# Kernel optimization log

Hardware: AMD Instinct MI355X
Metric: run time of the kernel (lower is better)

The kernel has to match this reference:

```python
import jax, jax.numpy as jnp
import numpy as np

B, S, E, H, DK = 2, 1024, 1024, 128, 8  # batch, seq, embed_dim, num_heads, d_k (= n_wires)


def setup_inputs() -> dict:
    key = jax.random.key(0)
    ks = jax.random.split(key, 10)
    sc = 1.0 / np.sqrt(E)
    inp = {
        "x": jax.random.normal(ks[0], (B, S, E), dtype=jnp.float32),
        "Wq": jax.random.normal(ks[1], (E, E), dtype=jnp.float32) * sc,
        "bq": jnp.zeros((E,), jnp.float32),
        "Wk": jax.random.normal(ks[2], (E, E), dtype=jnp.float32) * sc,
        "bk": jnp.zeros((E,), jnp.float32),
        "Wv": jax.random.normal(ks[3], (E, E), dtype=jnp.float32) * sc,
        "bv": jnp.zeros((E,), jnp.float32),
        "phi": jax.random.uniform(ks[4], (H, DK), jnp.float32, -np.pi, np.pi),  # trainable RX angles per head
        "Wo": jax.random.normal(ks[5], (E, E), dtype=jnp.float32) * sc,
        "bo": jnp.zeros((E,), jnp.float32),
    }
    return inp


def reference(x, Wq, bq, Wk, bk, Wv, bv, phi, Wo, bo):
    b, s, e = x.shape
    h, dk = phi.shape
    # QKV projections (k, v are computed but unused in the original forward)
    q = (x @ Wq.T + bq).reshape(b, s, h, dk).transpose(0, 2, 1, 3)  # [B,H,S,DK]
    k = (x @ Wk.T + bk).reshape(b, s, h, dk).transpose(0, 2, 1, 3)
    v = (x @ Wv.T + bv).reshape(b, s, h, dk).transpose(0, 2, 1, 3)
    del k, v  # dead in original math
    # Quantum circuit per head: RX(q_i) then RX(phi_i) on |0>, measure PauliZ.
    # RX angles on same wire add; <Z> after RX(theta)|0> = cos(theta).
    out = jnp.cos(q + phi[None, :, None, :])  # [B,H,S,DK]
    scores = jnp.einsum("bhsd,bhtd->bhst", out, out) / np.sqrt(dk)
    attn = jax.nn.softmax(scores, axis=-1)  # dropout is identity in eval mode
    ctx = jnp.einsum("bhst,bhtd->bhsd", attn, out)
    ctx = ctx.transpose(0, 2, 1, 3).reshape(b, s, e)
    return ctx @ Wo.T + bo
```

## Files before the change

kernel.cpp:

```cpp
#include <hip/hip_runtime.h>
#include <hip/hip_bf16.h>

#define Bv  2
#define Sv  1024
#define Ev  1024
#define Hv  128
#define DKv 8
#define Mv  (Bv*Sv)

typedef __attribute__((ext_vector_type(8))) short short8;
typedef __attribute__((ext_vector_type(4))) float f32x4;

static __device__ __forceinline__ short f2b(float f) {
    __hip_bfloat16 h = __float2bfloat16(f);
    return *reinterpret_cast<short*>(&h);
}

static __device__ __forceinline__ unsigned cvtpk(float a, float b) {
    unsigned r;
    asm("v_cvt_pk_bf16_f32 %0, %1, %2" : "=v"(r) : "v"(a), "v"(b));
    return r;
}

static __device__ __forceinline__ float hexp2(float x) {
    return __builtin_amdgcn_exp2f(x);
}

static __device__ __forceinline__ void gload16(const void* g, void* l) {
    __builtin_amdgcn_global_load_lds(
        (const __attribute__((address_space(1))) unsigned int*)g,
        (__attribute__((address_space(3))) unsigned int*)l, 16, 0, 0);
}

__global__ __launch_bounds__(256)
void cvt_all(const float* __restrict__ x, const float* __restrict__ wq,
             const float* __restrict__ wo, short* __restrict__ xb,
             short* __restrict__ wqb, short* __restrict__ wob)
{
    const int b = blockIdx.x;
    const float* src; short* dst; int i;
    if (b < 1024)      { src = x;  dst = xb;  i = b * 256 + threadIdx.x; }
    else if (b < 1536) { src = wq; dst = wqb; i = (b - 1024) * 256 + threadIdx.x; }
    else               { src = wo; dst = wob; i = (b - 1536) * 256 + threadIdx.x; }
    float4 a = ((const float4*)src)[2 * i];
    float4 c = ((const float4*)src)[2 * i + 1];
    uint4 o;
    o.x = cvtpk(a.x, a.y); o.y = cvtpk(a.z, a.w);
    o.z = cvtpk(c.x, c.y); o.w = cvtpk(c.z, c.w);
    ((uint4*)dst)[i] = o;
}

template<int EPI>
__global__ __launch_bounds__(256)
void gemm_bf16(const short* __restrict__ A, const short* __restrict__ W,
               const float* __restrict__ bias, const float* __restrict__ phi,
               void* __restrict__ outv)
{
    __shared__ short As[2][64 * 64];
    __shared__ short Bs[2][64 * 64];

    const int t    = threadIdx.x;
    const int w    = t >> 6, lane = t & 63;
    const int c    = lane & 15, g = lane >> 4;
    const int cs   = c & 7;
    const int wr   = w >> 1,  wc = w & 1;
    const int tm   = blockIdx.y * 64, tn = blockIdx.x * 64;
    const int lr   = lane >> 3;
    const int lcs  = ((lane & 7) ^ lr) * 8;

    f32x4 acc[2][2] = {};

    #define STAGE(s, k0)                                                        \
        _Pragma("unroll")                                                       \
        for (int j = 0; j < 2; j++) {                                           \
            const int row = w * 16 + j * 8;                                     \
            gload16(&A[(size_t)(tm + row + lr) * Ev + (k0) + lcs], &As[s][row * 64]); \
            gload16(&W[(size_t)(tn + row + lr) * Ev + (k0) + lcs], &Bs[s][row * 64]); \
        }

    STAGE(0, 0)
    __syncthreads();

    for (int ks = 0; ks < 16; ks++) {
        const int cur = ks & 1;
        if (ks < 15) { STAGE(cur ^ 1, (ks + 1) * 64) }
        #pragma unroll
        for (int kk = 0; kk < 64; kk += 32) {
            const int s0 = ((kk >> 3) + g) ^ cs;
            short8 af[2], bf[2];
            #pragma unroll
            for (int m = 0; m < 2; m++)
                af[m] = *(const short8*)&As[cur][(wr * 32 + m * 16 + c) * 64 + s0 * 8];
            #pragma unroll
            for (int n = 0; n < 2; n++)
                bf[n] = *(const short8*)&Bs[cur][(wc * 32 + n * 16 + c) * 64 + s0 * 8];
            #pragma unroll
            for (int m = 0; m < 2; m++)
                #pragma unroll
                for (int n = 0; n < 2; n++)
                    acc[m][n] = __builtin_amdgcn_mfma_f32_16x16x32_bf16(af[m], bf[n], acc[m][n], 0, 0, 0);
        }
        __syncthreads();
    }

    #pragma unroll
    for (int i = 0; i < 2; i++) {
        #pragma unroll
        for (int j = 0; j < 2; j++) {
            const int n = tn + wc * 32 + j * 16 + c;
            #pragma unroll
            for (int r = 0; r < 4; r++) {
                const int m = tm + wr * 32 + i * 16 + 4 * g + r;
                const float v = acc[i][j][r];
                if (EPI == 0) {
                    float q = __cosf(v + bias[n] + phi[n]);
                    const int bb = m >> 10, ss = m & (Sv - 1);
                    const int hh = n >> 3,  dd = n & (DKv - 1);
                    ((short*)outv)[(((size_t)bb * Hv + hh) * Sv + ss) * DKv + dd] = f2b(q);
                } else {
                    ((float*)outv)[(size_t)m * Ev + n] = v + bias[n];
                }
            }
        }
    }
    #undef STAGE
}

__global__ __launch_bounds__(256)
void attn_mfma(const short* __restrict__ om, short* __restrict__ ctx)
{
    __shared__ short K_lds[Sv * DKv];
    __shared__ short Vt[DKv * 1032];
    __shared__ short P_lds[4][16][40];

    const int t  = threadIdx.x;
    const int bh = blockIdx.x;
    const short* base = om + (size_t)bh * (Sv * DKv);

    #pragma unroll
    for (int r = 0; r < 4; r++) {
        const int k = r * 256 + t;
        int4 row = ((const int4*)base)[k];
        ((int4*)K_lds)[k] = row;
        union { int4 v; short s[8]; } u; u.v = row;
        #pragma unroll
        for (int d = 0; d < 8; d++) Vt[d * 1032 + k] = u.s[d];
    }
    __syncthreads();

    const int w = t >> 6, lane = t & 63;
    const int c = lane & 15, g = lane >> 4;
    const int q0 = blockIdx.y * 64 + w * 16;

    short8 qf = {};
    if (g == 0) qf = *(const short8*)&K_lds[(q0 + c) * 8];

    f32x4 ctx_acc = {0.f, 0.f, 0.f, 0.f};
    float lsum = 0.f;

    for (int kt = 0; kt < Sv; kt += 32) {
        short8 kf0 = {}, kf1 = {};
        if (g == 0) {
            kf0 = *(const short8*)&K_lds[(kt +      c) * 8];
            kf1 = *(const short8*)&K_lds[(kt + 16 + c) * 8];
        }
        const f32x4 z = {0.f, 0.f, 0.f, 0.f};
        f32x4 s0 = __builtin_amdgcn_mfma_f32_16x16x32_bf16(kf0, qf, z, 0, 0, 0);
        f32x4 s1 = __builtin_amdgcn_mfma_f32_16x16x32_bf16(kf1, qf, z, 0, 0, 0);

        float p[8];
        #pragma unroll
        for (int r = 0; r < 4; r++) {
            p[r]     = hexp2(s0[r] * 0.5100697f);
            p[4 + r] = hexp2(s1[r] * 0.5100697f);
        }
        lsum += ((p[0] + p[1]) + (p[2] + p[3])) + ((p[4] + p[5]) + (p[6] + p[7]));

        uint2 w0, w1;
        w0.x = cvtpk(p[0], p[1]); w0.y = cvtpk(p[2], p[3]);
        w1.x = cvtpk(p[4], p[5]); w1.y = cvtpk(p[6], p[7]);
        *(uint2*)&P_lds[w][c][4 * g]      = w0;
        *(uint2*)&P_lds[w][c][16 + 4 * g] = w1;

        short8 pf = *(const short8*)&P_lds[w][c][8 * g];
        short8 vf = {};
        if (c < 8) vf = *(const short8*)&Vt[c * 1032 + kt + 8 * g];
        ctx_acc = __builtin_amdgcn_mfma_f32_16x16x32_bf16(pf, vf, ctx_acc, 0, 0, 0);
    }

    lsum += __shfl_xor(lsum, 16);
    lsum += __shfl_xor(lsum, 32);
    float L[4];
    #pragma unroll
    for (int r = 0; r < 4; r++) L[r] = __shfl(lsum, 4 * g + r);

    if (c < 8) {
        const int b = bh >> 7, h = bh & (Hv - 1);
        #pragma unroll
        for (int r = 0; r < 4; r++) {
            const int q = q0 + 4 * g + r;
            ctx[((size_t)(b * Sv + q)) * Ev + h * DKv + c] = f2b(ctx_acc[r] / L[r]);
        }
    }
}

extern "C" void kernel_launch(void* const* d_in, const int* in_sizes, int n_in,
                              void* d_out, int out_size, void* d_ws, size_t ws_size,
                              hipStream_t stream)
{
    const float* x   = (const float*)d_in[0];
    const float* Wq  = (const float*)d_in[1];
    const float* bq  = (const float*)d_in[2];
    const float* phi = (const float*)d_in[7];
    const float* Wo  = (const float*)d_in[8];
    const float* bo  = (const float*)d_in[9];
    float* out = (float*)d_out;

    char* ws = (char*)d_ws;
    short* xb  = (short*)ws;
    short* ctx = xb;
    short* om  = (short*)(ws + (4 << 20));
    short* Wqb = (short*)(ws + (8 << 20));
    short* Wob = (short*)(ws + (10 << 20));

    cvt_all<<<dim3(2048), 256, 0, stream>>>(x, Wq, Wo, xb, Wqb, Wob);

    const dim3 gg(Ev / 64, Mv / 64);
    gemm_bf16<0><<<gg, 256, 0, stream>>>(xb, Wqb, bq, phi, (void*)om);
    attn_mfma<<<dim3(Bv * Hv, Sv / 64), 256, 0, stream>>>(om, ctx);
    gemm_bf16<1><<<gg, 256, 0, stream>>>(ctx, Wob, bo, nullptr, (void*)out);
}
```

Before: 174.1 us.

## Fuse fp32-to-bf16 conversion into GEMM staging and fold softmax scale into cos

```diff
diff --git a/kernel.cpp b/kernel.cpp
--- a/kernel.cpp
+++ b/kernel.cpp
@@ -8,6 +8,9 @@
 #define DKv 8
 #define Mv  (Bv*Sv)
 
+#define SQC  0.7141916f
+#define ISQC 1.4001855f
+
 typedef __attribute__((ext_vector_type(8))) short short8;
 typedef __attribute__((ext_vector_type(4))) float f32x4;
 
@@ -32,29 +35,12 @@
         (__attribute__((address_space(3))) unsigned int*)l, 16, 0, 0);
 }
 
+template<int AF32, int WF32, int EPI>
 __global__ __launch_bounds__(256)
-void cvt_all(const float* __restrict__ x, const float* __restrict__ wq,
-             const float* __restrict__ wo, short* __restrict__ xb,
-             short* __restrict__ wqb, short* __restrict__ wob)
-{
-    const int b = blockIdx.x;
-    const float* src; short* dst; int i;
-    if (b < 1024)      { src = x;  dst = xb;  i = b * 256 + threadIdx.x; }
-    else if (b < 1536) { src = wq; dst = wqb; i = (b - 1024) * 256 + threadIdx.x; }
-    else               { src = wo; dst = wob; i = (b - 1536) * 256 + threadIdx.x; }
-    float4 a = ((const float4*)src)[2 * i];
-    float4 c = ((const float4*)src)[2 * i + 1];
-    uint4 o;
-    o.x = cvtpk(a.x, a.y); o.y = cvtpk(a.z, a.w);
-    o.z = cvtpk(c.x, c.y); o.w = cvtpk(c.z, c.w);
-    ((uint4*)dst)[i] = o;
-}
-
-template<int EPI>
-__global__ __launch_bounds__(256)
-void gemm_bf16(const short* __restrict__ A, const short* __restrict__ W,
+void gemm_bf16(const short* __restrict__ Ab, const float* __restrict__ Af,
+               const short* __restrict__ Wb, const float* __restrict__ Wf,
                const float* __restrict__ bias, const float* __restrict__ phi,
-               void* __restrict__ outv)
+               float wscale, void* __restrict__ outv)
 {
     __shared__ short As[2][64 * 64];
     __shared__ short Bs[2][64 * 64];
@@ -67,23 +53,67 @@
     const int tm   = blockIdx.y * 64, tn = blockIdx.x * 64;
     const int lr   = lane >> 3;
     const int lcs  = ((lane & 7) ^ lr) * 8;
+    const int rsr  = lane >> 1;
+    const int rsh  = lane & 1;
 
     f32x4 acc[2][2] = {};
 
-    #define STAGE(s, k0)                                                        \
-        _Pragma("unroll")                                                       \
-        for (int j = 0; j < 2; j++) {                                           \
-            const int row = w * 16 + j * 8;                                     \
-            gload16(&A[(size_t)(tm + row + lr) * Ev + (k0) + lcs], &As[s][row * 64]); \
-            gload16(&W[(size_t)(tn + row + lr) * Ev + (k0) + lcs], &Bs[s][row * 64]); \
-        }
-
-    STAGE(0, 0)
+    auto stage = [&](int s, int k0) {
+        if (w < 2) {
+            if constexpr (AF32) {
+                const int r = w * 32 + rsr;
+                const float* gp = &Af[(size_t)(tm + r) * Ev + k0 + rsh * 32];
+                float4 f[8];
+                #pragma unroll
+                for (int i = 0; i < 8; i++) f[i] = ((const float4*)gp)[i];
+                short* dst = &As[s][r * 64];
+                #pragma unroll
+                for (int i = 0; i < 4; i++) {
+                    uint4 u = { cvtpk(f[2*i].x,   f[2*i].y),
+                                cvtpk(f[2*i].z,   f[2*i].w),
+                                cvtpk(f[2*i+1].x, f[2*i+1].y),
+                                cvtpk(f[2*i+1].z, f[2*i+1].w) };
+                    *(uint4*)&dst[((rsh * 4 + i) ^ (r & 7)) * 8] = u;
+                }
+            } else {
+                #pragma unroll
+                for (int j = 0; j < 4; j++) {
+                    const int row = w * 32 + j * 8;
+                    gload16(&Ab[(size_t)(tm + row + lr) * Ev + k0 + lcs], &As[s][row * 64]);
+                }
+            }
+        } else {
+            if constexpr (WF32) {
+                const int r = (w - 2) * 32 + rsr;
+                const float* gp = &Wf[(size_t)(tn + r) * Ev + k0 + rsh * 32];
+                float4 f[8];
+                #pragma unroll
+                for (int i = 0; i < 8; i++) f[i] = ((const float4*)gp)[i];
+                short* dst = &Bs[s][r * 64];
+                #pragma unroll
+                for (int i = 0; i < 4; i++) {
+                    uint4 u = { cvtpk(f[2*i].x * wscale,   f[2*i].y * wscale),
+                                cvtpk(f[2*i].z * wscale,   f[2*i].w * wscale),
+                                cvtpk(f[2*i+1].x * wscale, f[2*i+1].y * wscale),
+                                cvtpk(f[2*i+1].z * wscale, f[2*i+1].w * wscale) };
+                    *(uint4*)&dst[((rsh * 4 + i) ^ (r & 7)) * 8] = u;
+                }
+            } else {
+                #pragma unroll
+                for (int j = 0; j < 4; j++) {
+                    const int row = (w - 2) * 32 + j * 8;
+                    gload16(&Wb[(size_t)(tn + row + lr) * Ev + k0 + lcs], &Bs[s][row * 64]);
+                }
+            }
+        }
+    };
+
+    stage(0, 0);
     __syncthreads();
 
     for (int ks = 0; ks < 16; ks++) {
         const int cur = ks & 1;
-        if (ks < 15) { STAGE(cur ^ 1, (ks + 1) * 64) }
+        if (ks < 15) stage(cur ^ 1, (ks + 1) * 64);
         #pragma unroll
         for (int kk = 0; kk < 64; kk += 32) {
             const int s0 = ((kk >> 3) + g) ^ cs;
@@ -113,7 +143,7 @@
                 const int m = tm + wr * 32 + i * 16 + 4 * g + r;
                 const float v = acc[i][j][r];
                 if (EPI == 0) {
-                    float q = __cosf(v + bias[n] + phi[n]);
+                    float q = __cosf(v + bias[n] + phi[n]) * SQC;
                     const int bb = m >> 10, ss = m & (Sv - 1);
                     const int hh = n >> 3,  dd = n & (DKv - 1);
                     ((short*)outv)[(((size_t)bb * Hv + hh) * Sv + ss) * DKv + dd] = f2b(q);
@@ -123,7 +153,6 @@
             }
         }
     }
-    #undef STAGE
 }
 
 __global__ __launch_bounds__(256)
@@ -171,8 +200,8 @@
         float p[8];
         #pragma unroll
         for (int r = 0; r < 4; r++) {
-            p[r]     = hexp2(s0[r] * 0.5100697f);
-            p[4 + r] = hexp2(s1[r] * 0.5100697f);
+            p[r]     = hexp2(s0[r]);
+            p[4 + r] = hexp2(s1[r]);
         }
         lsum += ((p[0] + p[1]) + (p[2] + p[3])) + ((p[4] + p[5]) + (p[6] + p[7]));
 
@@ -217,16 +246,13 @@
     float* out = (float*)d_out;
 
     char* ws = (char*)d_ws;
-    short* xb  = (short*)ws;
-    short* ctx = xb;
+    short* ctx = (short*)ws;
     short* om  = (short*)(ws + (4 << 20));
-    short* Wqb = (short*)(ws + (8 << 20));
-    short* Wob = (short*)(ws + (10 << 20));
-
-    cvt_all<<<dim3(2048), 256, 0, stream>>>(x, Wq, Wo, xb, Wqb, Wob);
 
     const dim3 gg(Ev / 64, Mv / 64);
-    gemm_bf16<0><<<gg, 256, 0, stream>>>(xb, Wqb, bq, phi, (void*)om);
+    gemm_bf16<1, 1, 0><<<gg, 256, 0, stream>>>(nullptr, x, nullptr, Wq,
+                                               bq, phi, 1.0f, (void*)om);
     attn_mfma<<<dim3(Bv * Hv, Sv / 64), 256, 0, stream>>>(om, ctx);
-    gemm_bf16<1><<<gg, 256, 0, stream>>>(ctx, Wob, bo, nullptr, (void*)out);
-}
+    gemm_bf16<0, 1, 1><<<gg, 256, 0, stream>>>(ctx, nullptr, nullptr, Wo,
+                                               bo, nullptr, ISQC, (void*)out);
+}
```

After: 186.3 us. 1.07x slower.
